# Kernel optimization log

Measured on AMD Instinct MI355X. Metric: run time of the kernel, lower is better.

The kernel has to match this reference:

```python
import jax, jax.numpy as jnp
import numpy as np

HASH_BUCKETS = 1000
EMB_DIM = 16
LSTM_UNITS = 32
DENSE_UNITS = 32


def setup_inputs() -> dict:
    key = jax.random.key(0)
    ks = jax.random.split(key, 8)
    B, T = 4096, 512
    ids = jax.random.randint(ks[0], (B, T), 0, HASH_BUCKETS, dtype=jnp.int32)
    emb = jax.random.normal(ks[1], (HASH_BUCKETS, EMB_DIM), jnp.float32) * 0.05
    kernel = jax.random.normal(ks[2], (EMB_DIM, 4 * LSTM_UNITS), jnp.float32) * 0.1
    rec_kernel = jax.random.normal(ks[3], (LSTM_UNITS, 4 * LSTM_UNITS), jnp.float32) * 0.1
    w1 = jax.random.normal(ks[4], (LSTM_UNITS, DENSE_UNITS), jnp.float32) * 0.1
    b1 = jnp.zeros((DENSE_UNITS,), jnp.float32)
    w2 = jax.random.normal(ks[5], (DENSE_UNITS, 1), jnp.float32) * 0.1
    b2 = jnp.zeros((1,), jnp.float32)
    return {"ids": ids, "emb": emb, "kernel": kernel, "rec_kernel": rec_kernel,
            "w1": w1, "b1": b1, "w2": w2, "b2": b2}


def _lstm(x, kernel, rec_kernel):
    # x: [B, T, E]; Keras LSTM, use_bias=False, return last hidden state [B, H]
    B = x.shape[0]
    H = rec_kernel.shape[0]
    # precompute input projections for all timesteps: [T, B, 4H]
    xz = jnp.einsum('bte,ef->tbf', x, kernel)

    def step(carry, xz_t):
        h, c = carry
        z = xz_t + h @ rec_kernel  # [B, 4H]
        zi, zf, zc, zo = jnp.split(z, 4, axis=-1)  # Keras gate order i,f,c,o
        i = jax.nn.sigmoid(zi)
        f = jax.nn.sigmoid(zf)
        c = f * c + i * jnp.tanh(zc)
        o = jax.nn.sigmoid(zo)
        h = o * jnp.tanh(c)
        return (h, c), None

    init = (jnp.zeros((B, H), x.dtype), jnp.zeros((B, H), x.dtype))
    (h, _), _ = jax.lax.scan(step, init, xz)
    return h


def reference(ids, emb, kernel, rec_kernel, w1, b1, w2, b2):
    x = emb[ids]                        # [B, T, E] embedding lookup
    h = _lstm(x, kernel, rec_kernel)    # [B, H]
    y = jax.nn.relu(h @ w1 + b1)        # [B, 32]
    return y @ w2 + b2                  # [B, 1]
```

## Files before the change

### kernel.cpp

```cpp
#include <hip/hip_runtime.h>
#include <stdint.h>

#define HASH_BUCKETS 1000
#define EMB_DIM 16
#define HDIM 32
#define G4 128
#define TSTEPS 512
#define BATCH 4096
#define RSTRIDE 40

typedef short v8s __attribute__((ext_vector_type(8)));
typedef float v4f __attribute__((ext_vector_type(4)));

__device__ __forceinline__ float frcp(float x) {
    float r; asm("v_rcp_f32 %0, %1" : "=v"(r) : "v"(x)); return r;
}
__device__ __forceinline__ float fexp2(float x) {
    float r; asm("v_exp_f32 %0, %1" : "=v"(r) : "v"(x)); return r;
}
__device__ __forceinline__ uint32_t cvtpk_bf16(float a, float b) {
    uint32_t r; asm("v_cvt_pk_bf16_f32 %0, %1, %2" : "=v"(r) : "v"(a), "v"(b)); return r;
}
__device__ __forceinline__ uint32_t bf16rne(float x) {
    uint32_t u = __float_as_uint(x);
    return (u + 0x7FFFu + ((u >> 16) & 1u)) >> 16;
}

__global__ void precompute_P2_kernel(const float* __restrict__ emb,
                                     const float* __restrict__ kern,
                                     float* __restrict__ P2) {
    int idx = blockIdx.x * blockDim.x + threadIdx.x;
    if (idx >= HASH_BUCKETS * G4) return;
    int row = idx >> 7;
    int c2  = idx & 127;
    int h = c2 >> 2;
    int g = c2 & 3;
    float acc = 0.f;
#pragma unroll
    for (int e = 0; e < EMB_DIM; ++e)
        acc = fmaf(emb[row * EMB_DIM + e], kern[e * G4 + g * 32 + h], acc);
    float sg = (g == 2) ? 2.8853900817779268f : -1.4426950408889634f;
    P2[idx] = acc * sg;
}

__global__ __launch_bounds__(512)
__attribute__((amdgpu_waves_per_eu(2)))
void lstm_head_kernel(const int* __restrict__ ids,
                      const float* __restrict__ P2,
                      const float* __restrict__ R,
                      const float* __restrict__ w1,
                      const float* __restrict__ b1,
                      const float* __restrict__ w2,
                      const float* __restrict__ b2,
                      float* __restrict__ out) {
    __shared__ __align__(16) uint32_t hbuf[2][16][RSTRIDE];
    __shared__ float hfin[16][33];

    const int tid  = threadIdx.x;
    const int w    = tid >> 6;
    const int lane = tid & 63;
    const int col  = lane & 15;
    const int quad = lane >> 4;
    const int bb   = blockIdx.x * 16;
    const int unit = 4 * w + quad;
    const int sw   = (col ^ (col >> 2)) & 3;

    const float PL2E   =  2.8853900817779268f;
    const float NL2E   = -1.4426950408889634f;
    const float N2PL2E = -5.7707801635558536f;

    union V8 { uint32_t u[4]; v8s v; };
    V8 Ahi, Alo;
    {
        int tt = col >> 2, g = col & 3;
        float sg = (g == 2) ? PL2E : NL2E;
        int gc = g * 32 + 4 * w + tt;
#pragma unroll
        for (int r = 0; r < 4; ++r) {
            uint32_t hp[2], lp[2];
#pragma unroll
            for (int e = 0; e < 2; ++e) {
                int k = quad * 8 + r + 4 * e;
                float x = R[k * G4 + gc] * sg;
                uint32_t hb = bf16rne(x);
                hp[e] = hb;
                lp[e] = bf16rne(x - __uint_as_float(hb << 16));
            }
            Ahi.u[r] = hp[0] | (hp[1] << 16);
            Alo.u[r] = lp[0] | (lp[1] << 16);
        }
    }

    for (int i = tid; i < 2 * 16 * RSTRIDE; i += 512)
        ((uint32_t*)hbuf)[i] = 0u;

    const uint32_t* rdH[2] = { &hbuf[0][col][4 * (quad ^ sw)],
                               &hbuf[1][col][4 * (quad ^ sw)] };
    uint16_t* base16 = (uint16_t*)&hbuf[0][0][0];
    const int bufhalf = 16 * RSTRIDE * 2;
    {
    }
    const int hidw = col * RSTRIDE + 4 * (((w >> 1)) ^ sw) + quad;
    const int h16  = hidw * 2 + (w & 1);
    const int l16  = h16 + 32;
    uint16_t* wrH[2] = { base16 + bufhalf + h16, base16 + h16 };
    uint16_t* wrL[2] = { base16 + bufhalf + l16, base16 + l16 };

    const int* __restrict__ idrow = ids + (size_t)(bb + col) * TSTEPS;
    int ida = idrow[0];
    float4 xz_c = *(const float4*)(P2 + (size_t)ida * G4 + 4 * unit);
    int idb = idrow[1];
    float4 xz_n = *(const float4*)(P2 + (size_t)idb * G4 + 4 * unit);
    int id_c = idrow[2];
    int id_n = idrow[3];

    float cc = 0.f, hv = 0.f;
    const v4f vzero = {0.f, 0.f, 0.f, 0.f};

    __syncthreads();

    union V8R { uint4 q; v8s v; };

#define STEP(PB, T)                                                             \
    {                                                                           \
                                  \
        V8R Bhi, Blo;                                                           \
        Bhi.q = *(const uint4*)(rdH[PB]);                                       \
        Blo.q = *(const uint4*)(rdH[PB] + 16);                                  \
                     \
        float4 xz_f = *(const float4*)(P2 + (size_t)id_c * G4 + 4 * unit);      \
        int id_f = idrow[((T) + 4 < TSTEPS) ? ((T) + 4) : (TSTEPS - 1)];        \
        v4f xzv = {xz_c.x, xz_c.y, xz_c.z, xz_c.w};                             \
        v4f ma = __builtin_amdgcn_mfma_f32_16x16x32_bf16(Alo.v, Bhi.v, vzero, 0, 0, 0); \
        v4f mb = __builtin_amdgcn_mfma_f32_16x16x32_bf16(Ahi.v, Blo.v, vzero, 0, 0, 0); \
        v4f mc = __builtin_amdgcn_mfma_f32_16x16x32_bf16(Ahi.v, Bhi.v, xzv, 0, 0, 0);   \
        v4f z = (ma + mb) + mc;                                                 \
                                               \
        float di = 1.f + fexp2(z[0]);                                           \
        float df = 1.f + fexp2(z[1]);                                           \
        float dc = 1.f + fexp2(z[2]);                                           \
        float dq = 1.f + fexp2(z[3]);                                           \
        float Pp = di * df, Qq = dc * dq;                                       \
        float rr = frcp(Pp * Qq);                                               \
        float rP = rr * Qq, rQ = rr * Pp;                                       \
        float ig = rP * df, fg = rP * di, rc = rQ * dq, og = rQ * dc;           \
        float tz = fmaf(N2PL2E, rc, PL2E);                   \
        cc = fmaf(fg, cc, ig * tz);                \
        float tc = fmaf(-2.f, frcp(1.f + fexp2(cc)), 1.f);                      \
        hv = og * tc;                                                           \
                               \
        uint32_t th = cvtpk_bf16(hv, hv);                                       \
        wrH[PB][0] = (uint16_t)th;                                              \
        float lo = hv - __uint_as_float(th << 16);                              \
        uint32_t tl = cvtpk_bf16(lo, lo);                                       \
        wrL[PB][0] = (uint16_t)tl;                                              \
        xz_c = xz_n; xz_n = xz_f;                                               \
        id_c = id_n; id_n = id_f;                                               \
                                               \
        asm volatile("s_waitcnt lgkmcnt(0)\n\ts_barrier" ::: "memory");         \
    }

    for (int t = 0; t < TSTEPS; t += 2) {
        STEP(0, t)
        STEP(1, t + 1)
    }
#undef STEP

    hfin[col][unit] = hv;
    __syncthreads();

    int u  = tid & 31;
    int bq = tid >> 5;
    {
        float y = b1[u];
#pragma unroll
        for (int k = 0; k < HDIM; ++k)
            y = fmaf(hfin[bq][k], w1[k * HDIM + u], y);
        y = fmaxf(y, 0.f);
        float vv = y * w2[u];
#pragma unroll
        for (int off = 16; off >= 1; off >>= 1)
            vv += __shfl_xor(vv, off);
        if (u == 0) out[bb + bq] = vv + b2[0];
    }
}

extern "C" void kernel_launch(void* const* d_in, const int* in_sizes, int n_in,
                              void* d_out, int out_size, void* d_ws, size_t ws_size,
                              hipStream_t stream) {
    const int*   ids  = (const int*)d_in[0];
    const float* emb  = (const float*)d_in[1];
    const float* kern = (const float*)d_in[2];
    const float* rec  = (const float*)d_in[3];
    const float* w1   = (const float*)d_in[4];
    const float* b1   = (const float*)d_in[5];
    const float* w2   = (const float*)d_in[6];
    const float* b2   = (const float*)d_in[7];
    float* out = (float*)d_out;
    float* P2  = (float*)d_ws;

    precompute_P2_kernel<<<(HASH_BUCKETS * G4 + 255) / 256, 256, 0, stream>>>(
        emb, kern, P2);
    lstm_head_kernel<<<BATCH / 16, 512, 0, stream>>>(
        ids, P2, rec, w1, b1, w2, b2, out);
}
```

Before: 299.4 us.

## Run LSTM recurrence in a single wavefront with register-resident hidden state

Replaces the 8-wave block, which exchanged the hidden state through shared memory with a barrier every timestep, by one 64-lane wave per 16-sample block. Each wave holds all recurrent weights as 8 bf16 hi/lo MFMA fragments in registers, and the new hidden state is packed straight into the next step's B operand. This removes the per-step LDS round trip and s_barrier. The cost is 24 serial MFMAs and 8x the gate math per wave each step, far higher register pressure, and only 256 single-wave blocks to cover the GPU.

Result: slower. 494.2 us (+65.1%).

```diff
diff --git a/kernel.cpp b/kernel.cpp
--- a/kernel.cpp
+++ b/kernel.cpp
@@ -7,7 +7,6 @@
 #define G4 128
 #define TSTEPS 512
 #define BATCH 4096
-#define RSTRIDE 40
 
 typedef short v8s __attribute__((ext_vector_type(8)));
 typedef float v4f __attribute__((ext_vector_type(4)));
@@ -43,8 +42,8 @@
     P2[idx] = acc * sg;
 }
 
-__global__ __launch_bounds__(512)
-__attribute__((amdgpu_waves_per_eu(2)))
+__global__ __launch_bounds__(64)
+__attribute__((amdgpu_waves_per_eu(1, 1)))
 void lstm_head_kernel(const int* __restrict__ ids,
                       const float* __restrict__ P2,
                       const float* __restrict__ R,
@@ -53,125 +52,141 @@
                       const float* __restrict__ w2,
                       const float* __restrict__ b2,
                       float* __restrict__ out) {
-    __shared__ __align__(16) uint32_t hbuf[2][16][RSTRIDE];
     __shared__ float hfin[16][33];
 
-    const int tid  = threadIdx.x;
-    const int w    = tid >> 6;
-    const int lane = tid & 63;
+    const int lane = threadIdx.x & 63;
     const int col  = lane & 15;
-    const int quad = lane >> 4;
+    const int q    = lane >> 4;
     const int bb   = blockIdx.x * 16;
-    const int unit = 4 * w + quad;
-    const int sw   = (col ^ (col >> 2)) & 3;
 
     const float PL2E   =  2.8853900817779268f;
     const float NL2E   = -1.4426950408889634f;
     const float N2PL2E = -5.7707801635558536f;
 
     union V8 { uint32_t u[4]; v8s v; };
-    V8 Ahi, Alo;
+    V8 Ahi[8], Alo[8];
     {
-        int tt = col >> 2, g = col & 3;
-        float sg = (g == 2) ? PL2E : NL2E;
-        int gc = g * 32 + 4 * w + tt;
-#pragma unroll
-        for (int r = 0; r < 4; ++r) {
-            uint32_t hp[2], lp[2];
-#pragma unroll
-            for (int e = 0; e < 2; ++e) {
-                int k = quad * 8 + r + 4 * e;
-                float x = R[k * G4 + gc] * sg;
-                uint32_t hb = bf16rne(x);
-                hp[e] = hb;
-                lp[e] = bf16rne(x - __uint_as_float(hb << 16));
+        const int arow = col;
+        const int r  = arow & 3;
+        const int qp = arow >> 2;
+        const float sg = (r == 2) ? PL2E : NL2E;
+#pragma unroll
+        for (int j = 0; j < 8; ++j) {
+            const int gcol = r * 32 + 8 * qp + j;
+#pragma unroll
+            for (int d = 0; d < 4; ++d) {
+                uint32_t hp[2], lp[2];
+#pragma unroll
+                for (int e = 0; e < 2; ++e) {
+                    int k = 8 * q + 2 * d + e;
+                    float x = R[k * G4 + gcol] * sg;
+                    uint32_t hb = bf16rne(x);
+                    hp[e] = hb;
+                    lp[e] = bf16rne(x - __uint_as_float(hb << 16));
+                }
+                Ahi[j].u[d] = hp[0] | (hp[1] << 16);
+                Alo[j].u[d] = lp[0] | (lp[1] << 16);
             }
-            Ahi.u[r] = hp[0] | (hp[1] << 16);
-            Alo.u[r] = lp[0] | (lp[1] << 16);
         }
     }
 
-    for (int i = tid; i < 2 * 16 * RSTRIDE; i += 512)
-        ((uint32_t*)hbuf)[i] = 0u;
-
-    const uint32_t* rdH[2] = { &hbuf[0][col][4 * (quad ^ sw)],
-                               &hbuf[1][col][4 * (quad ^ sw)] };
-    uint16_t* base16 = (uint16_t*)&hbuf[0][0][0];
-    const int bufhalf = 16 * RSTRIDE * 2;
+    V8 Bhi, Blo;
+#pragma unroll
+    for (int d = 0; d < 4; ++d) { Bhi.u[d] = 0u; Blo.u[d] = 0u; }
+    float cc[8], hv[8];
+#pragma unroll
+    for (int j = 0; j < 8; ++j) { cc[j] = 0.f; hv[j] = 0.f; }
+
+    const int* __restrict__ idrow = ids + (size_t)(bb + col) * TSTEPS;
+    const float* __restrict__ pbase = P2;
+    v4f xzE[8], xzO[8];
     {
-    }
-    const int hidw = col * RSTRIDE + 4 * (((w >> 1)) ^ sw) + quad;
-    const int h16  = hidw * 2 + (w & 1);
-    const int l16  = h16 + 32;
-    uint16_t* wrH[2] = { base16 + bufhalf + h16, base16 + h16 };
-    uint16_t* wrL[2] = { base16 + bufhalf + l16, base16 + l16 };
-
-    const int* __restrict__ idrow = ids + (size_t)(bb + col) * TSTEPS;
-    int ida = idrow[0];
-    float4 xz_c = *(const float4*)(P2 + (size_t)ida * G4 + 4 * unit);
-    int idb = idrow[1];
-    float4 xz_n = *(const float4*)(P2 + (size_t)idb * G4 + 4 * unit);
-    int id_c = idrow[2];
-    int id_n = idrow[3];
-
-    float cc = 0.f, hv = 0.f;
-    const v4f vzero = {0.f, 0.f, 0.f, 0.f};
-
+        const float* p0 = pbase + (size_t)idrow[0] * G4 + 32 * q;
+        const float* p1 = pbase + (size_t)idrow[1] * G4 + 32 * q;
+#pragma unroll
+        for (int j = 0; j < 8; ++j) xzE[j] = *(const v4f*)(p0 + 4 * j);
+#pragma unroll
+        for (int j = 0; j < 8; ++j) xzO[j] = *(const v4f*)(p1 + 4 * j);
+    }
+    int idE = idrow[2];
+    int idO = idrow[3];
+
+#define STEP(XZ, IDX, T)                                                        \
+    {                                                                           \
+                         \
+        v4f z0_ = __builtin_amdgcn_mfma_f32_16x16x32_bf16(Ahi[0].v, Bhi.v, XZ[0], 0, 0, 0); \
+        v4f z1_ = __builtin_amdgcn_mfma_f32_16x16x32_bf16(Ahi[1].v, Bhi.v, XZ[1], 0, 0, 0); \
+        v4f z2_ = __builtin_amdgcn_mfma_f32_16x16x32_bf16(Ahi[2].v, Bhi.v, XZ[2], 0, 0, 0); \
+        v4f z3_ = __builtin_amdgcn_mfma_f32_16x16x32_bf16(Ahi[3].v, Bhi.v, XZ[3], 0, 0, 0); \
+        v4f z4_ = __builtin_amdgcn_mfma_f32_16x16x32_bf16(Ahi[4].v, Bhi.v, XZ[4], 0, 0, 0); \
+        v4f z5_ = __builtin_amdgcn_mfma_f32_16x16x32_bf16(Ahi[5].v, Bhi.v, XZ[5], 0, 0, 0); \
+        v4f z6_ = __builtin_amdgcn_mfma_f32_16x16x32_bf16(Ahi[6].v, Bhi.v, XZ[6], 0, 0, 0); \
+        v4f z7_ = __builtin_amdgcn_mfma_f32_16x16x32_bf16(Ahi[7].v, Bhi.v, XZ[7], 0, 0, 0); \
+                       \
+        {                                                                       \
+            const float* pf_ = pbase + (size_t)(IDX) * G4 + 32 * q;             \
+            _Pragma("unroll")                                                   \
+            for (int j = 0; j < 8; ++j) XZ[j] = *(const v4f*)(pf_ + 4 * j);     \
+        }                                                                       \
+        IDX = idrow[((T) + 4 < TSTEPS) ? ((T) + 4) : (TSTEPS - 1)];             \
+        z0_ = __builtin_amdgcn_mfma_f32_16x16x32_bf16(Alo[0].v, Bhi.v, z0_, 0, 0, 0); \
+        z1_ = __builtin_amdgcn_mfma_f32_16x16x32_bf16(Alo[1].v, Bhi.v, z1_, 0, 0, 0); \
+        z2_ = __builtin_amdgcn_mfma_f32_16x16x32_bf16(Alo[2].v, Bhi.v, z2_, 0, 0, 0); \
+        z3_ = __builtin_amdgcn_mfma_f32_16x16x32_bf16(Alo[3].v, Bhi.v, z3_, 0, 0, 0); \
+        z4_ = __builtin_amdgcn_mfma_f32_16x16x32_bf16(Alo[4].v, Bhi.v, z4_, 0, 0, 0); \
+        z5_ = __builtin_amdgcn_mfma_f32_16x16x32_bf16(Alo[5].v, Bhi.v, z5_, 0, 0, 0); \
+        z6_ = __builtin_amdgcn_mfma_f32_16x16x32_bf16(Alo[6].v, Bhi.v, z6_, 0, 0, 0); \
+        z7_ = __builtin_amdgcn_mfma_f32_16x16x32_bf16(Alo[7].v, Bhi.v, z7_, 0, 0, 0); \
+        z0_ = __builtin_amdgcn_mfma_f32_16x16x32_bf16(Ahi[0].v, Blo.v, z0_, 0, 0, 0); \
+        z1_ = __builtin_amdgcn_mfma_f32_16x16x32_bf16(Ahi[1].v, Blo.v, z1_, 0, 0, 0); \
+        z2_ = __builtin_amdgcn_mfma_f32_16x16x32_bf16(Ahi[2].v, Blo.v, z2_, 0, 0, 0); \
+        z3_ = __builtin_amdgcn_mfma_f32_16x16x32_bf16(Ahi[3].v, Blo.v, z3_, 0, 0, 0); \
+        z4_ = __builtin_amdgcn_mfma_f32_16x16x32_bf16(Ahi[4].v, Blo.v, z4_, 0, 0, 0); \
+        z5_ = __builtin_amdgcn_mfma_f32_16x16x32_bf16(Ahi[5].v, Blo.v, z5_, 0, 0, 0); \
+        z6_ = __builtin_amdgcn_mfma_f32_16x16x32_bf16(Ahi[6].v, Blo.v, z6_, 0, 0, 0); \
+        z7_ = __builtin_amdgcn_mfma_f32_16x16x32_bf16(Ahi[7].v, Blo.v, z7_, 0, 0, 0); \
+        v4f zz[8] = { z0_, z1_, z2_, z3_, z4_, z5_, z6_, z7_ };                 \
+        _Pragma("unroll")                                                       \
+        for (int j = 0; j < 8; ++j) {                                           \
+            float di = 1.f + fexp2(zz[j][0]);                                   \
+            float df = 1.f + fexp2(zz[j][1]);                                   \
+            float dc = 1.f + fexp2(zz[j][2]);                                   \
+            float dq = 1.f + fexp2(zz[j][3]);                                   \
+            float Pp = di * df, Qq = dc * dq;                                   \
+            float rr = frcp(Pp * Qq);                                           \
+            float rP = rr * Qq, rQ = rr * Pp;                                   \
+            float ig = rP * df, fg = rP * di, rc = rQ * dq, og = rQ * dc;       \
+            float tz = fmaf(N2PL2E, rc, PL2E);               \
+            cc[j] = fmaf(fg, cc[j], ig * tz);             \
+            float tc = fmaf(-2.f, frcp(1.f + fexp2(cc[j])), 1.f);               \
+            hv[j] = og * tc;                                                    \
+        }                                                                       \
+                  \
+        _Pragma("unroll")                                                       \
+        for (int d = 0; d < 4; ++d) {                                           \
+            uint32_t ph = cvtpk_bf16(hv[2 * d], hv[2 * d + 1]);                 \
+            Bhi.u[d] = ph;                                                      \
+            float lo0 = hv[2 * d]     - __uint_as_float(ph << 16);              \
+            float lo1 = hv[2 * d + 1] - __uint_as_float(ph & 0xffff0000u);      \
+            Blo.u[d] = cvtpk_bf16(lo0, lo1);                                    \
+        }                                                                       \
+    }
+
+    for (int t = 0; t < TSTEPS; t += 2) {
+        STEP(xzE, idE, t)
+        STEP(xzO, idO, t + 1)
+    }
+#undef STEP
+
+#pragma unroll
+    for (int j = 0; j < 8; ++j)
+        hfin[col][8 * q + j] = hv[j];
     __syncthreads();
 
-    union V8R { uint4 q; v8s v; };
-
-#define STEP(PB, T)                                                             \
-    {                                                                           \
-                                  \
-        V8R Bhi, Blo;                                                           \
-        Bhi.q = *(const uint4*)(rdH[PB]);                                       \
-        Blo.q = *(const uint4*)(rdH[PB] + 16);                                  \
-                     \
-        float4 xz_f = *(const float4*)(P2 + (size_t)id_c * G4 + 4 * unit);      \
-        int id_f = idrow[((T) + 4 < TSTEPS) ? ((T) + 4) : (TSTEPS - 1)];        \
-        v4f xzv = {xz_c.x, xz_c.y, xz_c.z, xz_c.w};                             \
-        v4f ma = __builtin_amdgcn_mfma_f32_16x16x32_bf16(Alo.v, Bhi.v, vzero, 0, 0, 0); \
-        v4f mb = __builtin_amdgcn_mfma_f32_16x16x32_bf16(Ahi.v, Blo.v, vzero, 0, 0, 0); \
-        v4f mc = __builtin_amdgcn_mfma_f32_16x16x32_bf16(Ahi.v, Bhi.v, xzv, 0, 0, 0);   \
-        v4f z = (ma + mb) + mc;                                                 \
-                                               \
-        float di = 1.f + fexp2(z[0]);                                           \
-        float df = 1.f + fexp2(z[1]);                                           \
-        float dc = 1.f + fexp2(z[2]);                                           \
-        float dq = 1.f + fexp2(z[3]);                                           \
-        float Pp = di * df, Qq = dc * dq;                                       \
-        float rr = frcp(Pp * Qq);                                               \
-        float rP = rr * Qq, rQ = rr * Pp;                                       \
-        float ig = rP * df, fg = rP * di, rc = rQ * dq, og = rQ * dc;           \
-        float tz = fmaf(N2PL2E, rc, PL2E);                   \
-        cc = fmaf(fg, cc, ig * tz);                \
-        float tc = fmaf(-2.f, frcp(1.f + fexp2(cc)), 1.f);                      \
-        hv = og * tc;                                                           \
-                               \
-        uint32_t th = cvtpk_bf16(hv, hv);                                       \
-        wrH[PB][0] = (uint16_t)th;                                              \
-        float lo = hv - __uint_as_float(th << 16);                              \
-        uint32_t tl = cvtpk_bf16(lo, lo);                                       \
-        wrL[PB][0] = (uint16_t)tl;                                              \
-        xz_c = xz_n; xz_n = xz_f;                                               \
-        id_c = id_n; id_n = id_f;                                               \
-                                               \
-        asm volatile("s_waitcnt lgkmcnt(0)\n\ts_barrier" ::: "memory");         \
-    }
-
-    for (int t = 0; t < TSTEPS; t += 2) {
-        STEP(0, t)
-        STEP(1, t + 1)
-    }
-#undef STEP
-
-    hfin[col][unit] = hv;
-    __syncthreads();
-
-    int u  = tid & 31;
-    int bq = tid >> 5;
-    {
+    const int u = lane & 31;
+#pragma unroll
+    for (int it = 0; it < 8; ++it) {
+        int bq = (lane >> 5) + 2 * it;
         float y = b1[u];
 #pragma unroll
         for (int k = 0; k < HDIM; ++k)
@@ -201,6 +216,6 @@
 
     precompute_P2_kernel<<<(HASH_BUCKETS * G4 + 255) / 256, 256, 0, stream>>>(
         emb, kern, P2);
-    lstm_head_kernel<<<BATCH / 16, 512, 0, stream>>>(
+    lstm_head_kernel<<<BATCH / 16, 64, 0, stream>>>(
         ids, P2, rec, w1, b1, w2, b2, out);
 }
```
